# Kernel optimization log

Hardware: AMD Instinct MI355X
Metric: run time of the kernel (lower is better)

The kernel has to match this reference:

```python
import jax, jax.numpy as jnp
from jax import lax
import numpy as np

INPUT_SIZE, HIDDEN, NUM_LAYERS, OUTPUT = 64, 512, 2, 1024
BATCH, SEQ = 64, 1024


def setup_inputs() -> dict:
    key = jax.random.key(0)
    ks = jax.random.split(key, 11)
    s = 1.0 / np.sqrt(HIDDEN)
    u = lambda k, shape: jax.random.uniform(k, shape, jnp.float32, -s, s)
    return {
        "x": jax.random.normal(ks[0], (BATCH, SEQ, INPUT_SIZE), jnp.float32),
        # layer 0 (PyTorch gate order: i, f, g, o stacked along dim 0)
        "W_ih0": u(ks[1], (4 * HIDDEN, INPUT_SIZE)),
        "W_hh0": u(ks[2], (4 * HIDDEN, HIDDEN)),
        "b_ih0": u(ks[3], (4 * HIDDEN,)),
        "b_hh0": u(ks[4], (4 * HIDDEN,)),
        # layer 1
        "W_ih1": u(ks[5], (4 * HIDDEN, HIDDEN)),
        "W_hh1": u(ks[6], (4 * HIDDEN, HIDDEN)),
        "b_ih1": u(ks[7], (4 * HIDDEN,)),
        "b_hh1": u(ks[8], (4 * HIDDEN,)),
        # fc
        "fc_w": u(ks[9], (OUTPUT, HIDDEN)),
        "fc_b": u(ks[10], (OUTPUT,)),
    }


def _lstm_layer(x, W_ih, W_hh, b_ih, b_hh):
    # x: [B, T, D]. Precompute input projection for all timesteps (one big GEMM).
    B = x.shape[0]
    H = W_hh.shape[1]
    xw = jnp.einsum('btd,gd->btg', x, W_ih) + b_ih + b_hh  # [B, T, 4H]
    xw = jnp.swapaxes(xw, 0, 1)  # [T, B, 4H] for scan
    h0 = jnp.zeros((B, H), x.dtype)
    c0 = jnp.zeros((B, H), x.dtype)

    def step(carry, xw_t):
        h, c = carry
        gates = xw_t + h @ W_hh.T  # [B, 4H]
        i, f, g, o = jnp.split(gates, 4, axis=-1)
        c = jax.nn.sigmoid(f) * c + jax.nn.sigmoid(i) * jnp.tanh(g)
        h = jax.nn.sigmoid(o) * jnp.tanh(c)
        return (h, c), h

    (h_T, c_T), hs = lax.scan(step, (h0, c0), xw)
    return jnp.swapaxes(hs, 0, 1), h_T  # [B, T, H], [B, H]


def _forward(x, W_ih0, W_hh0, b_ih0, b_hh0, W_ih1, W_hh1, b_ih1, b_hh1, fc_w, fc_b):
    ula0, h0_T = _lstm_layer(x, W_ih0, W_hh0, b_ih0, b_hh0)
    ula1, h1_T = _lstm_layer(ula0, W_ih1, W_hh1, b_ih1, b_hh1)
    # h_out: [num_layers, B, H] -> view(-1, H)
    h_out = jnp.concatenate([h0_T, h1_T], axis=0)  # [L*B, H]
    out = h_out @ fc_w.T + fc_b
    out = jax.nn.relu(out)
    # Dropout(p=0.2): identity in eval mode (deterministic reference)
    return out


def reference(x, W_ih0, W_hh0, b_ih0, b_hh0, W_ih1, W_hh1, b_ih1, b_hh1, fc_w, fc_b):
    return _forward(x, W_ih0, W_hh0, b_ih0, b_hh0, W_ih1, W_hh1, b_ih1, b_hh1, fc_w, fc_b)
```

## Files before the change

### kernel.cpp

```cpp
#include <hip/hip_runtime.h>


#define H      512
#define T_SEQ  1024
#define DIN    64
#define STEPS  1025

#define SLOT_U32 16384
#define GRP_U32  49152
#define WS_BYTES (4 * GRP_U32 * 4)

typedef _Float16 f16x8 __attribute__((ext_vector_type(8)));
typedef float    f32x4 __attribute__((ext_vector_type(4)));

__device__ __forceinline__ unsigned long long ld_u64(const unsigned long long* p) {
  return __hip_atomic_load((unsigned long long*)p, __ATOMIC_RELAXED, __HIP_MEMORY_SCOPE_AGENT);
}
__device__ __forceinline__ void st_u32(unsigned* p, unsigned v) {
  __hip_atomic_store(p, v, __ATOMIC_RELAXED, __HIP_MEMORY_SCOPE_AGENT);
}
__device__ __forceinline__ f16x8 pk8(float4 a, float4 b) {
  f16x8 r;
  r[0] = (_Float16)a.x; r[1] = (_Float16)a.y; r[2] = (_Float16)a.z; r[3] = (_Float16)a.w;
  r[4] = (_Float16)b.x; r[5] = (_Float16)b.y; r[6] = (_Float16)b.z; r[7] = (_Float16)b.w;
  return r;
}
__device__ __forceinline__ f16x8 cvt8(const float* p) {
  return pk8(*(const float4*)p, *(const float4*)(p + 4));
}
__device__ __forceinline__ f32x4 mfma16(f16x8 a, f16x8 b, f32x4 c) {
  return __builtin_amdgcn_mfma_f32_16x16x32_f16(a, b, c, 0, 0, 0);
}
__device__ __forceinline__ float rcpf_(float x) {
#if __has_builtin(__builtin_amdgcn_rcpf)
  return __builtin_amdgcn_rcpf(x);
#else
  return 1.0f / x;
#endif
}
__device__ __forceinline__ float sigm(float x) {
  x = fminf(fmaxf(x, -30.f), 30.f);
  return rcpf_(1.f + __expf(-x));
}
__device__ __forceinline__ float tanhx(float x) {
  x = fminf(fmaxf(x, -15.f), 15.f);
  float e = __expf(2.f * x);
  return (e - 1.f) * rcpf_(e + 1.f);
}

__global__ __launch_bounds__(256, 1)
void lstm_fused(const float* __restrict__ x,
                const float* __restrict__ Wih0, const float* __restrict__ Whh0,
                const float* __restrict__ bih0, const float* __restrict__ bhh0,
                const float* __restrict__ Wih1, const float* __restrict__ Whh1,
                const float* __restrict__ bih1, const float* __restrict__ bhh1,
                const float* __restrict__ fcw,  const float* __restrict__ fcb,
                float* __restrict__ out, unsigned* __restrict__ ws)
{
  __shared__ unsigned sH[2][8320];

  const int tid  = threadIdx.x;
  const int wid  = blockIdx.x;
  const int g    = wid >> 5;
  const int w    = wid & 31;
  const int wv   = tid >> 6;
  const int lane = tid & 63;
  const int bcol = lane & 15;
  const int kgrp = lane >> 4;
  const int layer = wv >> 1;
  const int hb    = w * 16 + (wv & 1) * 8;

  unsigned* gbase = ws + g * GRP_U32;

  const int src_m = lane & 15;
  const int gr0 = (src_m & 3) * H + hb + (src_m >> 2);
  const int gr1 = gr0 + 4;
  f16x8 wA[2][32];
  if (layer == 0) {
    #pragma unroll
    for (int f = 0; f < 18; ++f) {
      const float *p0, *p1;
      if (f < 2) {
        p0 = Wih0 + (size_t)gr0 * DIN + f * 32 + kgrp * 8;
        p1 = Wih0 + (size_t)gr1 * DIN + f * 32 + kgrp * 8;
      } else {
        p0 = Whh0 + (size_t)gr0 * H + (f - 2) * 32 + kgrp * 8;
        p1 = Whh0 + (size_t)gr1 * H + (f - 2) * 32 + kgrp * 8;
      }
      wA[0][f] = cvt8(p0); wA[1][f] = cvt8(p1);
    }
  } else {
    #pragma unroll
    for (int f = 0; f < 16; ++f) {
      int col = f * 32 + kgrp * 8;
      wA[0][f] = cvt8(Wih1 + (size_t)gr0 * H + col);
      wA[1][f] = cvt8(Wih1 + (size_t)gr1 * H + col);
    }
    #pragma unroll
    for (int f = 16; f < 32; ++f) {
      int col = (f - 16) * 32 + kgrp * 8;
      wA[0][f] = cvt8(Whh1 + (size_t)gr0 * H + col);
      wA[1][f] = cvt8(Whh1 + (size_t)gr1 * H + col);
    }
  }
  float bias[2][4];
  {
    const float* bi = layer ? bih1 : bih0;
    const float* bh = layer ? bhh1 : bhh0;
    #pragma unroll
    for (int t = 0; t < 2; ++t)
      #pragma unroll
      for (int r = 0; r < 4; ++r) {
        int u = hb + t * 4 + kgrp;
        bias[t][r] = bi[r * H + u] + bh[r * H + u];
      }
  }

  for (int i = tid; i < 2 * 8320; i += 256) ((unsigned*)sH)[i] = 0;
  __syncthreads();

  float cst0 = 0.f, cst1 = 0.f;
  unsigned spins = 0;
  const int rowb = bcol * 1040 + kgrp * 16;

  for (int s = 0; s < STEPS; ++s) {
    float4 xr0 = {0,0,0,0}, xr1 = xr0, xr2 = xr0, xr3 = xr0;
    if (layer == 0) {
      int t = (s < T_SEQ) ? s : (T_SEQ - 1);
      const float* xp = x + ((size_t)((g * 16 + bcol) * T_SEQ + t)) * DIN + kgrp * 8;
      xr0 = *(const float4*)xp;        xr1 = *(const float4*)(xp + 4);
      xr2 = *(const float4*)(xp + 32); xr3 = *(const float4*)(xp + 36);
    }
    if (s > 0) {
      const unsigned long long* src =
          (const unsigned long long*)(gbase + ((s - 1) % 3) * SLOT_U32);
      const unsigned want = (unsigned)s;
      unsigned* dstbuf = sH[s & 1];
      #pragma unroll
      for (int pass = 0; pass < 2; ++pass) {
        unsigned long long v[16];
        #pragma unroll
        for (int i = 0; i < 16; ++i)
          v[i] = ld_u64(src + tid + (pass * 16 + i) * 256);
        for (;;) {
          unsigned bad = 0;
          #pragma unroll
          for (int i = 0; i < 16; ++i) {
            unsigned lo = (unsigned)v[i], hi = (unsigned)(v[i] >> 32);
            if (((lo >> 16) ^ want) | ((hi >> 16) ^ want)) bad |= (1u << i);
          }
          if (!bad) break;
          if (++spins > 8000000u) break;
          #pragma unroll
          for (int i = 0; i < 16; ++i)
            if (bad & (1u << i))
              v[i] = ld_u64(src + tid + (pass * 16 + i) * 256);
        }
        #pragma unroll
        for (int i = 0; i < 16; ++i) {
          int j = tid + (pass * 16 + i) * 256;
          unsigned payload = ((unsigned)v[i] & 0xffffu)
                           | ((unsigned)(v[i] >> 32) << 16);
          dstbuf[(j >> 12) * 4160 + ((j >> 8) & 15) * 260 + (j & 255)] = payload;
        }
      }
    }
    __syncthreads();

    const bool act = layer ? (s > 0) : (s < T_SEQ);
    float hv0 = 0.f, hv1 = 0.f;
    if (act) {
      f32x4 acc0 = {0,0,0,0}, acc1 = {0,0,0,0};
      const char* cur = (const char*)sH[s & 1];
      if (layer == 0) {
        f16x8 b0 = pk8(xr0, xr1);
        acc0 = mfma16(wA[0][0], b0, acc0); acc1 = mfma16(wA[1][0], b0, acc1);
        f16x8 b1 = pk8(xr2, xr3);
        acc0 = mfma16(wA[0][1], b1, acc0); acc1 = mfma16(wA[1][1], b1, acc1);
        #pragma unroll
        for (int f = 2; f < 18; ++f) {
          f16x8 bf = *(const f16x8*)(cur + rowb + (f - 2) * 64);
          acc0 = mfma16(wA[0][f], bf, acc0); acc1 = mfma16(wA[1][f], bf, acc1);
        }
      } else {
        #pragma unroll
        for (int f = 0; f < 16; ++f) {
          f16x8 bf = *(const f16x8*)(cur + rowb + f * 64);
          acc0 = mfma16(wA[0][f], bf, acc0); acc1 = mfma16(wA[1][f], bf, acc1);
        }
        #pragma unroll
        for (int f = 16; f < 32; ++f) {
          f16x8 bf = *(const f16x8*)(cur + 16640 + rowb + (f - 16) * 64);
          acc0 = mfma16(wA[0][f], bf, acc0); acc1 = mfma16(wA[1][f], bf, acc1);
        }
      }
      {
        float ii = sigm(acc0[0] + bias[0][0]);
        float ff = sigm(acc0[1] + bias[0][1]);
        float gg = tanhx(acc0[2] + bias[0][2]);
        float oo = sigm(acc0[3] + bias[0][3]);
        cst0 = ff * cst0 + ii * gg;
        hv0 = oo * tanhx(cst0);
      }
      {
        float ii = sigm(acc1[0] + bias[1][0]);
        float ff = sigm(acc1[1] + bias[1][1]);
        float gg = tanhx(acc1[2] + bias[1][2]);
        float oo = sigm(acc1[3] + bias[1][3]);
        cst1 = ff * cst1 + ii * gg;
        hv1 = oo * tanhx(cst1);
      }
    }
    const bool produce = layer ? true : (s < T_SEQ);
    if (produce) {
      unsigned tag = (unsigned)(s + 1) << 16;
      unsigned u0 = (unsigned)__builtin_bit_cast(unsigned short, (_Float16)hv0);
      unsigned u1 = (unsigned)__builtin_bit_cast(unsigned short, (_Float16)hv1);
      unsigned* dst = gbase + (s % 3) * SLOT_U32 + layer * 8192
                    + bcol * 512 + hb + kgrp;
      st_u32(dst,     u0 | tag);
      st_u32(dst + 4, u1 | tag);
    }
  }

  __syncthreads();

  {
    const int rt = wid >> 4, ct = wid & 15;
    const int sg = rt & 3;
    const bool isH1 = (rt >= 4);
    const unsigned want = isH1 ? (unsigned)STEPS : (unsigned)(STEPS - 1);
    const int     slot  = isH1 ? 1 : 0;
    const unsigned long long* src =
        (const unsigned long long*)(ws + sg * GRP_U32 + slot * SLOT_U32
                                    + (isH1 ? 8192 : 0));
    unsigned long long v[16];
    #pragma unroll
    for (int i = 0; i < 16; ++i) v[i] = ld_u64(src + tid + i * 256);
    for (;;) {
      unsigned bad = 0;
      #pragma unroll
      for (int i = 0; i < 16; ++i) {
        unsigned lo = (unsigned)v[i], hi = (unsigned)(v[i] >> 32);
        if (((lo >> 16) ^ want) | ((hi >> 16) ^ want)) bad |= (1u << i);
      }
      if (!bad) break;
      if (++spins > 8000000u) break;
      #pragma unroll
      for (int i = 0; i < 16; ++i)
        if (bad & (1u << i)) v[i] = ld_u64(src + tid + i * 256);
    }
    #pragma unroll
    for (int i = 0; i < 16; ++i) {
      int j = tid + i * 256;
      unsigned payload = ((unsigned)v[i] & 0xffffu)
                       | ((unsigned)(v[i] >> 32) << 16);
      sH[0][(j >> 8) * 260 + (j & 255)] = payload;
    }
    __syncthreads();
    const int col = ct * 64 + wv * 16 + bcol;
    f32x4 a0 = {0,0,0,0}, a1 = {0,0,0,0};
    #pragma unroll
    for (int f = 0; f < 16; ++f) {
      f16x8 af = *(const f16x8*)((const char*)sH[0] + rowb + f * 64);
      f16x8 bf = cvt8(fcw + (size_t)col * H + f * 32 + kgrp * 8);
      if (f & 1) a1 = mfma16(af, bf, a1); else a0 = mfma16(af, bf, a0);
    }
    f32x4 a = a0 + a1;
    const float fb = fcb[col];
    #pragma unroll
    for (int r = 0; r < 4; ++r) {
      int row = rt * 16 + kgrp * 4 + r;
      float v2 = a[r] + fb;
      out[(size_t)row * 1024 + col] = v2 > 0.f ? v2 : 0.f;
    }
  }
}

extern "C" void kernel_launch(void* const* d_in, const int* in_sizes, int n_in,
                              void* d_out, int out_size, void* d_ws, size_t ws_size,
                              hipStream_t stream) {
  const float* x    = (const float*)d_in[0];
  const float* Wih0 = (const float*)d_in[1];
  const float* Whh0 = (const float*)d_in[2];
  const float* bih0 = (const float*)d_in[3];
  const float* bhh0 = (const float*)d_in[4];
  const float* Wih1 = (const float*)d_in[5];
  const float* Whh1 = (const float*)d_in[6];
  const float* bih1 = (const float*)d_in[7];
  const float* bhh1 = (const float*)d_in[8];
  const float* fcw  = (const float*)d_in[9];
  const float* fcb  = (const float*)d_in[10];
  (void)in_sizes; (void)n_in; (void)out_size; (void)ws_size;

  hipMemsetAsync(d_ws, 0, WS_BYTES, stream);
  lstm_fused<<<dim3(128), dim3(256), 0, stream>>>(
      x, Wih0, Whh0, bih0, bhh0, Wih1, Whh1, bih1, bhh1, fcw, fcb,
      (float*)d_out, (unsigned*)d_ws);
}
```

Measured before the change: 4.221 ms.

## Split LSTM layers onto separate blocks with decoupled deeper ring buffers

```diff
diff --git a/kernel.cpp b/kernel.cpp
--- a/kernel.cpp
+++ b/kernel.cpp
@@ -4,17 +4,24 @@
 #define H      512
 #define T_SEQ  1024
 #define DIN    64
-#define STEPS  1025
-
-#define SLOT_U32 16384
-#define GRP_U32  49152
+
+#define D0       5
+#define D1       3
+#define H0_SLOT  8192
+#define H1_OFF   40960
+#define PROG_OFF 65536
+#define GRP_U32  65792
 #define WS_BYTES (4 * GRP_U32 * 4)
 
 typedef _Float16 f16x8 __attribute__((ext_vector_type(8)));
 typedef float    f32x4 __attribute__((ext_vector_type(4)));
-
-__device__ __forceinline__ unsigned long long ld_u64(const unsigned long long* p) {
-  return __hip_atomic_load((unsigned long long*)p, __ATOMIC_RELAXED, __HIP_MEMORY_SCOPE_AGENT);
+typedef unsigned long long u64t;
+
+__device__ __forceinline__ u64t ld_u64(const u64t* p) {
+  return __hip_atomic_load((u64t*)p, __ATOMIC_RELAXED, __HIP_MEMORY_SCOPE_AGENT);
+}
+__device__ __forceinline__ unsigned ld_u32a(const unsigned* p) {
+  return __hip_atomic_load((unsigned*)p, __ATOMIC_RELAXED, __HIP_MEMORY_SCOPE_AGENT);
 }
 __device__ __forceinline__ void st_u32(unsigned* p, unsigned v) {
   __hip_atomic_store(p, v, __ATOMIC_RELAXED, __HIP_MEMORY_SCOPE_AGENT);
@@ -46,6 +53,9 @@
   x = fminf(fmaxf(x, -15.f), 15.f);
   float e = __expf(2.f * x);
   return (e - 1.f) * rcpf_(e + 1.f);
+}
+__device__ __forceinline__ unsigned payload(u64t v) {
+  return ((unsigned)v & 0xffffu) | ((unsigned)(v >> 32) << 16);
 }
 
 __global__ __launch_bounds__(256, 1)
@@ -57,26 +67,27 @@
                 const float* __restrict__ fcw,  const float* __restrict__ fcb,
                 float* __restrict__ out, unsigned* __restrict__ ws)
 {
-  __shared__ unsigned sH[2][8320];
+  __shared__ unsigned sH[2 * 8320];
 
   const int tid  = threadIdx.x;
-  const int wid  = blockIdx.x;
-  const int g    = wid >> 5;
-  const int w    = wid & 31;
+  const int r    = blockIdx.x;
+  const int g    = blockIdx.y;
   const int wv   = tid >> 6;
   const int lane = tid & 63;
   const int bcol = lane & 15;
   const int kgrp = lane >> 4;
-  const int layer = wv >> 1;
-  const int hb    = w * 16 + (wv & 1) * 8;
+  const bool isL0 = (r < 16);
 
   unsigned* gbase = ws + g * GRP_U32;
+  unsigned* prog  = gbase + PROG_OFF;
 
   const int src_m = lane & 15;
+  const int hb = isL0 ? (r * 32 + wv * 8) : ((r - 16) * 16 + wv * 4);
   const int gr0 = (src_m & 3) * H + hb + (src_m >> 2);
-  const int gr1 = gr0 + 4;
-  f16x8 wA[2][32];
-  if (layer == 0) {
+
+  f16x8 wA[36];
+  if (isL0) {
+    const int gr1 = gr0 + 4;
     #pragma unroll
     for (int f = 0; f < 18; ++f) {
       const float *p0, *p1;
@@ -87,61 +98,47 @@
         p0 = Whh0 + (size_t)gr0 * H + (f - 2) * 32 + kgrp * 8;
         p1 = Whh0 + (size_t)gr1 * H + (f - 2) * 32 + kgrp * 8;
       }
-      wA[0][f] = cvt8(p0); wA[1][f] = cvt8(p1);
+      wA[f] = cvt8(p0); wA[18 + f] = cvt8(p1);
     }
   } else {
     #pragma unroll
-    for (int f = 0; f < 16; ++f) {
-      int col = f * 32 + kgrp * 8;
-      wA[0][f] = cvt8(Wih1 + (size_t)gr0 * H + col);
-      wA[1][f] = cvt8(Wih1 + (size_t)gr1 * H + col);
-    }
-    #pragma unroll
-    for (int f = 16; f < 32; ++f) {
-      int col = (f - 16) * 32 + kgrp * 8;
-      wA[0][f] = cvt8(Whh1 + (size_t)gr0 * H + col);
-      wA[1][f] = cvt8(Whh1 + (size_t)gr1 * H + col);
-    }
+    for (int f = 0; f < 16; ++f)
+      wA[f] = cvt8(Wih1 + (size_t)gr0 * H + f * 32 + kgrp * 8);
+    #pragma unroll
+    for (int f = 0; f < 16; ++f)
+      wA[16 + f] = cvt8(Whh1 + (size_t)gr0 * H + f * 32 + kgrp * 8);
   }
-  float bias[2][4];
+  float bias0[4], bias1[4];
   {
-    const float* bi = layer ? bih1 : bih0;
-    const float* bh = layer ? bhh1 : bhh0;
-    #pragma unroll
-    for (int t = 0; t < 2; ++t)
-      #pragma unroll
-      for (int r = 0; r < 4; ++r) {
-        int u = hb + t * 4 + kgrp;
-        bias[t][r] = bi[r * H + u] + bh[r * H + u];
-      }
+    const float* bi = isL0 ? bih0 : bih1;
+    const float* bh = isL0 ? bhh0 : bhh1;
+    #pragma unroll
+    for (int rr = 0; rr < 4; ++rr) {
+      int u0 = hb + kgrp;
+      bias0[rr] = bi[rr * H + u0] + bh[rr * H + u0];
+      int u1 = hb + 4 + kgrp;
+      bias1[rr] = isL0 ? (bi[rr * H + u1] + bh[rr * H + u1]) : 0.f;
+    }
   }
 
-  for (int i = tid; i < 2 * 8320; i += 256) ((unsigned*)sH)[i] = 0;
+  for (int i = tid; i < 2 * 8320; i += 256) sH[i] = 0;
   __syncthreads();
 
-  float cst0 = 0.f, cst1 = 0.f;
   unsigned spins = 0;
   const int rowb = bcol * 1040 + kgrp * 16;
 
-  for (int s = 0; s < STEPS; ++s) {
-    float4 xr0 = {0,0,0,0}, xr1 = xr0, xr2 = xr0, xr3 = xr0;
-    if (layer == 0) {
-      int t = (s < T_SEQ) ? s : (T_SEQ - 1);
+  if (isL0) {
+    float c0 = 0.f, c1 = 0.f;
+    for (int t = 0; t < T_SEQ; ++t) {
       const float* xp = x + ((size_t)((g * 16 + bcol) * T_SEQ + t)) * DIN + kgrp * 8;
-      xr0 = *(const float4*)xp;        xr1 = *(const float4*)(xp + 4);
-      xr2 = *(const float4*)(xp + 32); xr3 = *(const float4*)(xp + 36);
-    }
-    if (s > 0) {
-      const unsigned long long* src =
-          (const unsigned long long*)(gbase + ((s - 1) % 3) * SLOT_U32);
-      const unsigned want = (unsigned)s;
-      unsigned* dstbuf = sH[s & 1];
-      #pragma unroll
-      for (int pass = 0; pass < 2; ++pass) {
-        unsigned long long v[16];
-        #pragma unroll
-        for (int i = 0; i < 16; ++i)
-          v[i] = ld_u64(src + tid + (pass * 16 + i) * 256);
+      float4 xr0 = *(const float4*)xp;        float4 xr1 = *(const float4*)(xp + 4);
+      float4 xr2 = *(const float4*)(xp + 32); float4 xr3 = *(const float4*)(xp + 36);
+      if (t > 0) {
+        const u64t* src = (const u64t*)(gbase + ((t - 1) % D0) * H0_SLOT);
+        const unsigned want = (unsigned)t;
+        u64t v[16];
+        #pragma unroll
+        for (int i = 0; i < 16; ++i) v[i] = ld_u64(src + tid + i * 256);
         for (;;) {
           unsigned bad = 0;
           #pragma unroll
@@ -150,91 +147,150 @@
             if (((lo >> 16) ^ want) | ((hi >> 16) ^ want)) bad |= (1u << i);
           }
           if (!bad) break;
-          if (++spins > 8000000u) break;
+          if (++spins > 4000000u) break;
           #pragma unroll
           for (int i = 0; i < 16; ++i)
-            if (bad & (1u << i))
-              v[i] = ld_u64(src + tid + (pass * 16 + i) * 256);
-        }
+            if (bad & (1u << i)) v[i] = ld_u64(src + tid + i * 256);
+        }
+        if (wv == 0) {
+          int pv = (lane < 32) ? (int)ld_u32a(prog + lane) : 0x7fffffff;
+          while (!__all(pv >= t - 4)) {
+            if (++spins > 4000000u) break;
+            if (lane < 32) pv = (int)ld_u32a(prog + lane);
+          }
+        }
+        unsigned* db = sH + (t & 1) * 8320;
         #pragma unroll
         for (int i = 0; i < 16; ++i) {
-          int j = tid + (pass * 16 + i) * 256;
-          unsigned payload = ((unsigned)v[i] & 0xffffu)
-                           | ((unsigned)(v[i] >> 32) << 16);
-          dstbuf[(j >> 12) * 4160 + ((j >> 8) & 15) * 260 + (j & 255)] = payload;
-        }
-      }
-    }
-    __syncthreads();
-
-    const bool act = layer ? (s > 0) : (s < T_SEQ);
-    float hv0 = 0.f, hv1 = 0.f;
-    if (act) {
-      f32x4 acc0 = {0,0,0,0}, acc1 = {0,0,0,0};
-      const char* cur = (const char*)sH[s & 1];
-      if (layer == 0) {
+          int j = tid + i * 256;
+          db[(j >> 8) * 260 + (j & 255)] = payload(v[i]);
+        }
+      }
+      __syncthreads();
+
+      const char* cur = (const char*)(sH + (t & 1) * 8320);
+      f32x4 a0 = {0,0,0,0}, a1 = {0,0,0,0};
+      {
         f16x8 b0 = pk8(xr0, xr1);
-        acc0 = mfma16(wA[0][0], b0, acc0); acc1 = mfma16(wA[1][0], b0, acc1);
+        a0 = mfma16(wA[0], b0, a0); a1 = mfma16(wA[18], b0, a1);
         f16x8 b1 = pk8(xr2, xr3);
-        acc0 = mfma16(wA[0][1], b1, acc0); acc1 = mfma16(wA[1][1], b1, acc1);
-        #pragma unroll
-        for (int f = 2; f < 18; ++f) {
-          f16x8 bf = *(const f16x8*)(cur + rowb + (f - 2) * 64);
-          acc0 = mfma16(wA[0][f], bf, acc0); acc1 = mfma16(wA[1][f], bf, acc1);
-        }
-      } else {
-        #pragma unroll
-        for (int f = 0; f < 16; ++f) {
-          f16x8 bf = *(const f16x8*)(cur + rowb + f * 64);
-          acc0 = mfma16(wA[0][f], bf, acc0); acc1 = mfma16(wA[1][f], bf, acc1);
-        }
-        #pragma unroll
-        for (int f = 16; f < 32; ++f) {
-          f16x8 bf = *(const f16x8*)(cur + 16640 + rowb + (f - 16) * 64);
-          acc0 = mfma16(wA[0][f], bf, acc0); acc1 = mfma16(wA[1][f], bf, acc1);
-        }
-      }
+        a0 = mfma16(wA[1], b1, a0); a1 = mfma16(wA[19], b1, a1);
+      }
+      #pragma unroll
+      for (int f = 2; f < 18; ++f) {
+        f16x8 bf = *(const f16x8*)(cur + rowb + (f - 2) * 64);
+        a0 = mfma16(wA[f], bf, a0); a1 = mfma16(wA[18 + f], bf, a1);
+      }
+      float hv0, hv1;
       {
-        float ii = sigm(acc0[0] + bias[0][0]);
-        float ff = sigm(acc0[1] + bias[0][1]);
-        float gg = tanhx(acc0[2] + bias[0][2]);
-        float oo = sigm(acc0[3] + bias[0][3]);
-        cst0 = ff * cst0 + ii * gg;
-        hv0 = oo * tanhx(cst0);
+        float ii = sigm(a0[0] + bias0[0]);
+        float ff = sigm(a0[1] + bias0[1]);
+        float gg = tanhx(a0[2] + bias0[2]);
+        float oo = sigm(a0[3] + bias0[3]);
+        c0 = ff * c0 + ii * gg;  hv0 = oo * tanhx(c0);
       }
       {
-        float ii = sigm(acc1[0] + bias[1][0]);
-        float ff = sigm(acc1[1] + bias[1][1]);
-        float gg = tanhx(acc1[2] + bias[1][2]);
-        float oo = sigm(acc1[3] + bias[1][3]);
-        cst1 = ff * cst1 + ii * gg;
-        hv1 = oo * tanhx(cst1);
-      }
-    }
-    const bool produce = layer ? true : (s < T_SEQ);
-    if (produce) {
-      unsigned tag = (unsigned)(s + 1) << 16;
+        float ii = sigm(a1[0] + bias1[0]);
+        float ff = sigm(a1[1] + bias1[1]);
+        float gg = tanhx(a1[2] + bias1[2]);
+        float oo = sigm(a1[3] + bias1[3]);
+        c1 = ff * c1 + ii * gg;  hv1 = oo * tanhx(c1);
+      }
+      unsigned tag = (unsigned)(t + 1) << 16;
       unsigned u0 = (unsigned)__builtin_bit_cast(unsigned short, (_Float16)hv0);
       unsigned u1 = (unsigned)__builtin_bit_cast(unsigned short, (_Float16)hv1);
-      unsigned* dst = gbase + (s % 3) * SLOT_U32 + layer * 8192
-                    + bcol * 512 + hb + kgrp;
+      unsigned* dst = gbase + (t % D0) * H0_SLOT + bcol * 512 + hb + kgrp;
       st_u32(dst,     u0 | tag);
       st_u32(dst + 4, u1 | tag);
     }
+  } else {
+    const int q = r - 16;
+    float c0 = 0.f;
+    for (int u = 0; u < T_SEQ; ++u) {
+      const u64t* s0 = (const u64t*)(gbase + (u % D0) * H0_SLOT);
+      const u64t* s1 = (const u64t*)(gbase + H1_OFF + ((u + 2) % D1) * H0_SLOT);
+      const unsigned w0 = (unsigned)(u + 1), w1 = (unsigned)u;
+      u64t v0[16], v1[16];
+      #pragma unroll
+      for (int i = 0; i < 16; ++i) v0[i] = ld_u64(s0 + tid + i * 256);
+      if (u > 0) {
+        #pragma unroll
+        for (int i = 0; i < 16; ++i) v1[i] = ld_u64(s1 + tid + i * 256);
+      }
+      for (;;) {
+        unsigned bad0 = 0, bad1 = 0;
+        #pragma unroll
+        for (int i = 0; i < 16; ++i) {
+          unsigned lo = (unsigned)v0[i], hi = (unsigned)(v0[i] >> 32);
+          if (((lo >> 16) ^ w0) | ((hi >> 16) ^ w0)) bad0 |= (1u << i);
+        }
+        if (u > 0) {
+          #pragma unroll
+          for (int i = 0; i < 16; ++i) {
+            unsigned lo = (unsigned)v1[i], hi = (unsigned)(v1[i] >> 32);
+            if (((lo >> 16) ^ w1) | ((hi >> 16) ^ w1)) bad1 |= (1u << i);
+          }
+        }
+        if (!(bad0 | bad1)) break;
+        if (++spins > 4000000u) break;
+        #pragma unroll
+        for (int i = 0; i < 16; ++i) {
+          if (bad0 & (1u << i)) v0[i] = ld_u64(s0 + tid + i * 256);
+          if (bad1 & (1u << i)) v1[i] = ld_u64(s1 + tid + i * 256);
+        }
+      }
+      unsigned* db = sH + (u & 1) * 8320;
+      #pragma unroll
+      for (int i = 0; i < 16; ++i) {
+        int j = tid + i * 256;
+        db[(j >> 8) * 260 + (j & 255)] = payload(v0[i]);
+      }
+      if (u > 0) {
+        #pragma unroll
+        for (int i = 0; i < 16; ++i) {
+          int j = tid + i * 256;
+          db[4160 + (j >> 8) * 260 + (j & 255)] = payload(v1[i]);
+        }
+      }
+      __syncthreads();
+      if (tid == 0) st_u32(prog + q, (unsigned)(u + 1));
+
+      const char* cur = (const char*)db;
+      f32x4 a0 = {0,0,0,0}, a1 = {0,0,0,0};
+      #pragma unroll
+      for (int f = 0; f < 16; ++f) {
+        f16x8 bf = *(const f16x8*)(cur + rowb + f * 64);
+        if (f & 1) a1 = mfma16(wA[f], bf, a1); else a0 = mfma16(wA[f], bf, a0);
+      }
+      #pragma unroll
+      for (int f = 0; f < 16; ++f) {
+        f16x8 bf = *(const f16x8*)(cur + 16640 + rowb + f * 64);
+        if (f & 1) a1 = mfma16(wA[16 + f], bf, a1); else a0 = mfma16(wA[16 + f], bf, a0);
+      }
+      f32x4 a = a0 + a1;
+      float ii = sigm(a[0] + bias0[0]);
+      float ff = sigm(a[1] + bias0[1]);
+      float gg = tanhx(a[2] + bias0[2]);
+      float oo = sigm(a[3] + bias0[3]);
+      c0 = ff * c0 + ii * gg;
+      float hv = oo * tanhx(c0);
+
+      unsigned tag = (unsigned)(u + 1) << 16;
+      unsigned hu = (unsigned)__builtin_bit_cast(unsigned short, (_Float16)hv);
+      unsigned* dst = gbase + H1_OFF + (u % D1) * H0_SLOT + bcol * 512 + hb + kgrp;
+      st_u32(dst, hu | tag);
+    }
   }
 
-  __syncthreads();
-
-  {
-    const int rt = wid >> 4, ct = wid & 15;
+  const int fid = g * 48 + r;
+  if (fid < 128) {
+    const int rt = fid >> 4, ct = fid & 15;
     const int sg = rt & 3;
     const bool isH1 = (rt >= 4);
-    const unsigned want = isH1 ? (unsigned)STEPS : (unsigned)(STEPS - 1);
-    const int     slot  = isH1 ? 1 : 0;
-    const unsigned long long* src =
-        (const unsigned long long*)(ws + sg * GRP_U32 + slot * SLOT_U32
-                                    + (isH1 ? 8192 : 0));
-    unsigned long long v[16];
+    const u64t* src = (const u64t*)(ws + sg * GRP_U32
+                                    + (isH1 ? (H1_OFF + 0 * H0_SLOT) : (3 * H0_SLOT)));
+    const unsigned want = (unsigned)T_SEQ;
+    u64t v[16];
     #pragma unroll
     for (int i = 0; i < 16; ++i) v[i] = ld_u64(src + tid + i * 256);
     for (;;) {
@@ -245,33 +301,33 @@
         if (((lo >> 16) ^ want) | ((hi >> 16) ^ want)) bad |= (1u << i);
       }
       if (!bad) break;
-      if (++spins > 8000000u) break;
+      if (++spins > 4000000u) break;
+      __builtin_amdgcn_s_sleep(1);
       #pragma unroll
       for (int i = 0; i < 16; ++i)
         if (bad & (1u << i)) v[i] = ld_u64(src + tid + i * 256);
     }
+    __syncthreads();
     #pragma unroll
     for (int i = 0; i < 16; ++i) {
       int j = tid + i * 256;
-      unsigned payload = ((unsigned)v[i] & 0xffffu)
-                       | ((unsigned)(v[i] >> 32) << 16);
-      sH[0][(j >> 8) * 260 + (j & 255)] = payload;
+      sH[(j >> 8) * 260 + (j & 255)] = payload(v[i]);
     }
     __syncthreads();
     const int col = ct * 64 + wv * 16 + bcol;
     f32x4 a0 = {0,0,0,0}, a1 = {0,0,0,0};
     #pragma unroll
     for (int f = 0; f < 16; ++f) {
-      f16x8 af = *(const f16x8*)((const char*)sH[0] + rowb + f * 64);
+      f16x8 af = *(const f16x8*)((const char*)sH + rowb + f * 64);
       f16x8 bf = cvt8(fcw + (size_t)col * H + f * 32 + kgrp * 8);
       if (f & 1) a1 = mfma16(af, bf, a1); else a0 = mfma16(af, bf, a0);
     }
     f32x4 a = a0 + a1;
     const float fb = fcb[col];
     #pragma unroll
-    for (int r = 0; r < 4; ++r) {
-      int row = rt * 16 + kgrp * 4 + r;
-      float v2 = a[r] + fb;
+    for (int rr = 0; rr < 4; ++rr) {
+      int row = rt * 16 + kgrp * 4 + rr;
+      float v2 = a[rr] + fb;
       out[(size_t)row * 1024 + col] = v2 > 0.f ? v2 : 0.f;
     }
   }
@@ -294,7 +350,7 @@
   (void)in_sizes; (void)n_in; (void)out_size; (void)ws_size;
 
   hipMemsetAsync(d_ws, 0, WS_BYTES, stream);
-  lstm_fused<<<dim3(128), dim3(256), 0, stream>>>(
+  lstm_fused<<<dim3(48, 4), dim3(256), 0, stream>>>(
       x, Wih0, Whh0, bih0, bhh0, Wih1, Whh1, bih1, bhh1, fcw, fcb,
       (float*)d_out, (unsigned*)d_ws);
 }
```

After: 4.539 ms. 7.5% more time.

## Split batch into 8 groups of 8 rows across 256 workgroups

Applied to the files above, without the earlier changes.

```diff
diff --git a/kernel.cpp b/kernel.cpp
--- a/kernel.cpp
+++ b/kernel.cpp
@@ -6,15 +6,16 @@
 #define DIN    64
 #define STEPS  1025
 
-#define SLOT_U32 16384
-#define GRP_U32  49152
-#define WS_BYTES (4 * GRP_U32 * 4)
+#define SLOT_U32 8192
+#define GRP_U32  24576
+#define WS_BYTES (8 * GRP_U32 * 4)
 
 typedef _Float16 f16x8 __attribute__((ext_vector_type(8)));
 typedef float    f32x4 __attribute__((ext_vector_type(4)));
-
-__device__ __forceinline__ unsigned long long ld_u64(const unsigned long long* p) {
-  return __hip_atomic_load((unsigned long long*)p, __ATOMIC_RELAXED, __HIP_MEMORY_SCOPE_AGENT);
+typedef unsigned long long u64t;
+
+__device__ __forceinline__ u64t ld_u64(const u64t* p) {
+  return __hip_atomic_load((u64t*)p, __ATOMIC_RELAXED, __HIP_MEMORY_SCOPE_AGENT);
 }
 __device__ __forceinline__ void st_u32(unsigned* p, unsigned v) {
   __hip_atomic_store(p, v, __ATOMIC_RELAXED, __HIP_MEMORY_SCOPE_AGENT);
@@ -46,6 +47,9 @@
   x = fminf(fmaxf(x, -15.f), 15.f);
   float e = __expf(2.f * x);
   return (e - 1.f) * rcpf_(e + 1.f);
+}
+__device__ __forceinline__ unsigned payload(u64t v) {
+  return ((unsigned)v & 0xffffu) | ((unsigned)(v >> 32) << 16);
 }
 
 __global__ __launch_bounds__(256, 1)
@@ -60,15 +64,14 @@
   __shared__ unsigned sH[2][8320];
 
   const int tid  = threadIdx.x;
-  const int wid  = blockIdx.x;
-  const int g    = wid >> 5;
-  const int w    = wid & 31;
+  const int r    = blockIdx.x;
+  const int g    = blockIdx.y;
   const int wv   = tid >> 6;
   const int lane = tid & 63;
   const int bcol = lane & 15;
   const int kgrp = lane >> 4;
   const int layer = wv >> 1;
-  const int hb    = w * 16 + (wv & 1) * 8;
+  const int hb    = r * 16 + (wv & 1) * 8;
 
   unsigned* gbase = ws + g * GRP_U32;
 
@@ -110,9 +113,9 @@
     #pragma unroll
     for (int t = 0; t < 2; ++t)
       #pragma unroll
-      for (int r = 0; r < 4; ++r) {
+      for (int rr = 0; rr < 4; ++rr) {
         int u = hb + t * 4 + kgrp;
-        bias[t][r] = bi[r * H + u] + bh[r * H + u];
+        bias[t][rr] = bi[rr * H + u] + bh[rr * H + u];
       }
   }
 
@@ -127,42 +130,35 @@
     float4 xr0 = {0,0,0,0}, xr1 = xr0, xr2 = xr0, xr3 = xr0;
     if (layer == 0) {
       int t = (s < T_SEQ) ? s : (T_SEQ - 1);
-      const float* xp = x + ((size_t)((g * 16 + bcol) * T_SEQ + t)) * DIN + kgrp * 8;
+      int b = g * 8 + (bcol & 7);
+      const float* xp = x + ((size_t)(b * T_SEQ + t)) * DIN + kgrp * 8;
       xr0 = *(const float4*)xp;        xr1 = *(const float4*)(xp + 4);
       xr2 = *(const float4*)(xp + 32); xr3 = *(const float4*)(xp + 36);
     }
     if (s > 0) {
-      const unsigned long long* src =
-          (const unsigned long long*)(gbase + ((s - 1) % 3) * SLOT_U32);
+      const u64t* src = (const u64t*)(gbase + ((s - 1) % 3) * SLOT_U32);
       const unsigned want = (unsigned)s;
-      unsigned* dstbuf = sH[s & 1];
-      #pragma unroll
-      for (int pass = 0; pass < 2; ++pass) {
-        unsigned long long v[16];
+      u64t v[16];
+      #pragma unroll
+      for (int i = 0; i < 16; ++i) v[i] = ld_u64(src + tid + i * 256);
+      for (;;) {
+        unsigned bad = 0;
+        #pragma unroll
+        for (int i = 0; i < 16; ++i) {
+          unsigned lo = (unsigned)v[i], hi = (unsigned)(v[i] >> 32);
+          if (((lo >> 16) ^ want) | ((hi >> 16) ^ want)) bad |= (1u << i);
+        }
+        if (!bad) break;
+        if (++spins > 8000000u) break;
         #pragma unroll
         for (int i = 0; i < 16; ++i)
-          v[i] = ld_u64(src + tid + (pass * 16 + i) * 256);
-        for (;;) {
-          unsigned bad = 0;
-          #pragma unroll
-          for (int i = 0; i < 16; ++i) {
-            unsigned lo = (unsigned)v[i], hi = (unsigned)(v[i] >> 32);
-            if (((lo >> 16) ^ want) | ((hi >> 16) ^ want)) bad |= (1u << i);
-          }
-          if (!bad) break;
-          if (++spins > 8000000u) break;
-          #pragma unroll
-          for (int i = 0; i < 16; ++i)
-            if (bad & (1u << i))
-              v[i] = ld_u64(src + tid + (pass * 16 + i) * 256);
-        }
-        #pragma unroll
-        for (int i = 0; i < 16; ++i) {
-          int j = tid + (pass * 16 + i) * 256;
-          unsigned payload = ((unsigned)v[i] & 0xffffu)
-                           | ((unsigned)(v[i] >> 32) << 16);
-          dstbuf[(j >> 12) * 4160 + ((j >> 8) & 15) * 260 + (j & 255)] = payload;
-        }
+          if (bad & (1u << i)) v[i] = ld_u64(src + tid + i * 256);
+      }
+      unsigned* db = sH[s & 1];
+      #pragma unroll
+      for (int i = 0; i < 16; ++i) {
+        int j = tid + i * 256;
+        db[(j >> 11) * 4160 + ((j >> 8) & 7) * 260 + (j & 255)] = payload(v[i]);
       }
     }
     __syncthreads();
@@ -212,11 +208,11 @@
       }
     }
     const bool produce = layer ? true : (s < T_SEQ);
-    if (produce) {
+    if (produce && bcol < 8) {
       unsigned tag = (unsigned)(s + 1) << 16;
       unsigned u0 = (unsigned)__builtin_bit_cast(unsigned short, (_Float16)hv0);
       unsigned u1 = (unsigned)__builtin_bit_cast(unsigned short, (_Float16)hv1);
-      unsigned* dst = gbase + (s % 3) * SLOT_U32 + layer * 8192
+      unsigned* dst = gbase + (s % 3) * SLOT_U32 + layer * 4096
                     + bcol * 512 + hb + kgrp;
       st_u32(dst,     u0 | tag);
       st_u32(dst + 4, u1 | tag);
@@ -225,18 +221,23 @@
 
   __syncthreads();
 
-  {
-    const int rt = wid >> 4, ct = wid & 15;
-    const int sg = rt & 3;
+  const int fid = g * 32 + r;
+  if (fid < 128) {
+    const int rt = fid >> 4, ct = fid & 15;
     const bool isH1 = (rt >= 4);
     const unsigned want = isH1 ? (unsigned)STEPS : (unsigned)(STEPS - 1);
     const int     slot  = isH1 ? 1 : 0;
-    const unsigned long long* src =
-        (const unsigned long long*)(ws + sg * GRP_U32 + slot * SLOT_U32
-                                    + (isH1 ? 8192 : 0));
-    unsigned long long v[16];
-    #pragma unroll
-    for (int i = 0; i < 16; ++i) v[i] = ld_u64(src + tid + i * 256);
+    const int     bt    = rt & 3;
+    u64t v[16];
+    #pragma unroll
+    for (int i = 0; i < 16; ++i) {
+      int j = tid + i * 256;
+      int row = j >> 8, pair = j & 255;
+      int gg = bt * 2 + (row >> 3);
+      const u64t* sp = (const u64t*)(ws + gg * GRP_U32 + slot * SLOT_U32
+                                     + (isH1 ? 4096 : 0));
+      v[i] = ld_u64(sp + (row & 7) * 256 + pair);
+    }
     for (;;) {
       unsigned bad = 0;
       #pragma unroll
@@ -248,14 +249,19 @@
       if (++spins > 8000000u) break;
       #pragma unroll
       for (int i = 0; i < 16; ++i)
-        if (bad & (1u << i)) v[i] = ld_u64(src + tid + i * 256);
+        if (bad & (1u << i)) {
+          int j = tid + i * 256;
+          int row = j >> 8, pair = j & 255;
+          int gg = bt * 2 + (row >> 3);
+          const u64t* sp = (const u64t*)(ws + gg * GRP_U32 + slot * SLOT_U32
+                                         + (isH1 ? 4096 : 0));
+          v[i] = ld_u64(sp + (row & 7) * 256 + pair);
+        }
     }
     #pragma unroll
     for (int i = 0; i < 16; ++i) {
       int j = tid + i * 256;
-      unsigned payload = ((unsigned)v[i] & 0xffffu)
-                       | ((unsigned)(v[i] >> 32) << 16);
-      sH[0][(j >> 8) * 260 + (j & 255)] = payload;
+      sH[0][(j >> 8) * 260 + (j & 255)] = payload(v[i]);
     }
     __syncthreads();
     const int col = ct * 64 + wv * 16 + bcol;
@@ -269,9 +275,9 @@
     f32x4 a = a0 + a1;
     const float fb = fcb[col];
     #pragma unroll
-    for (int r = 0; r < 4; ++r) {
-      int row = rt * 16 + kgrp * 4 + r;
-      float v2 = a[r] + fb;
+    for (int rr = 0; rr < 4; ++rr) {
+      int row = rt * 16 + kgrp * 4 + rr;
+      float v2 = a[rr] + fb;
       out[(size_t)row * 1024 + col] = v2 > 0.f ? v2 : 0.f;
     }
   }
@@ -294,7 +300,7 @@
   (void)in_sizes; (void)n_in; (void)out_size; (void)ws_size;
 
   hipMemsetAsync(d_ws, 0, WS_BYTES, stream);
-  lstm_fused<<<dim3(128), dim3(256), 0, stream>>>(
+  lstm_fused<<<dim3(32, 8), dim3(256), 0, stream>>>(
       x, Wih0, Whh0, bih0, bhh0, Wih1, Whh1, bih1, bhh1, fcw, fcb,
       (float*)d_out, (unsigned*)d_ws);
 }
```

Result: slower. 4.646 ms (+10.1%).
